# Performance work log

Measured on AMD Instinct MI355X. Metric: run time of the kernel, lower is better.

The kernel has to match this reference:

```python
import jax, jax.numpy as jnp
import numpy as np

HIDDEN = 1024
HEADS = 16
HEAD_DIM = HIDDEN // HEADS
SPARSITY_RATIO = 0.5


def setup_inputs() -> dict:
    key = jax.random.key(0)
    ks = jax.random.split(key, 6)
    B, S = 2, 2048
    # Xavier-uniform for square Linear weights: limit = sqrt(6/(fan_in+fan_out))
    lim = float(np.sqrt(6.0 / (HIDDEN + HIDDEN)))
    x = jax.random.normal(ks[0], (B, S, HIDDEN), dtype=jnp.float32)
    Wq = jax.random.uniform(ks[1], (HIDDEN, HIDDEN), minval=-lim, maxval=lim, dtype=jnp.float32)
    Wk = jax.random.uniform(ks[2], (HIDDEN, HIDDEN), minval=-lim, maxval=lim, dtype=jnp.float32)
    Wv = jax.random.uniform(ks[3], (HIDDEN, HIDDEN), minval=-lim, maxval=lim, dtype=jnp.float32)
    Wo = jax.random.uniform(ks[4], (HIDDEN, HIDDEN), minval=-lim, maxval=lim, dtype=jnp.float32)
    bo = jnp.zeros((HIDDEN,), dtype=jnp.float32)
    adaptive_threshold = jnp.asarray(0.1, dtype=jnp.float32)
    return {"x": x, "Wq": Wq, "Wk": Wk, "Wv": Wv, "Wo": Wo, "bo": bo,
            "adaptive_threshold": adaptive_threshold}


def reference(x, Wq, Wk, Wv, Wo, bo, adaptive_threshold):
    B, S, _ = x.shape
    H, D = HEADS, HEAD_DIM
    # projections (torch Linear: y = x @ W.T), split heads -> [B, H, S, D]
    q = (x @ Wq.T).reshape(B, S, H, D).transpose(0, 2, 1, 3)
    k = (x @ Wk.T).reshape(B, S, H, D).transpose(0, 2, 1, 3)
    v = (x @ Wv.T).reshape(B, S, H, D).transpose(0, 2, 1, 3)
    scores = jnp.einsum('bhqd,bhkd->bhqk', q, k) / jnp.sqrt(jnp.asarray(D, x.dtype))
    # adaptive top-k sparsity: keep top k entries per query row
    k_keep = max(1, int(S * (1.0 - SPARSITY_RATIO)))
    topv = jax.lax.top_k(scores, k_keep)[0]          # [B,H,S,k]
    kth = topv[..., -1:]                              # k-th largest per row
    thr = jnp.clip(adaptive_threshold, 0.0, 1.0)
    keep = (scores >= kth) & (scores >= thr)
    neg_inf = jnp.asarray(-jnp.inf, scores.dtype)
    masked = jnp.where(keep, scores, neg_inf)
    attn = jax.nn.softmax(masked, axis=-1)            # dropout is no-op in eval
    out = jnp.einsum('bhqk,bhkd->bhqd', attn, v)      # [B,H,S,D]
    out = out.transpose(0, 2, 1, 3).reshape(B, S, H * D)
    return out @ Wo.T + bo
```

## Files before the change

kernel.cpp:

```cpp
#include <hip/hip_runtime.h>
#include <hip/hip_bf16.h>
#include <cstdint>
#include <cstddef>

#define HIDDEN 1024
#define HEADS  16
#define HDIM   64
#define BATCH  2
#define SEQ    2048
#define MTOT   (BATCH*SEQ)
#define KSEL   1024
#define QT     16

typedef __attribute__((ext_vector_type(8))) short bf16x8;
typedef __attribute__((ext_vector_type(4))) float f32x4;

__device__ __forceinline__ unsigned short f2bf_rne(float f) {
    unsigned u = __float_as_uint(f);
    u += 0x7fffu + ((u >> 16) & 1u);
    return (unsigned short)(u >> 16);
}
__device__ __forceinline__ float bf2f(unsigned short h) {
    return __uint_as_float(((unsigned)h) << 16);
}
__device__ __forceinline__ int score_bucket(float v) {
    int b = (int)floorf(__fmaf_rn(v, 32.0f, 256.0f));
    return min(511, max(0, b));
}
__device__ __forceinline__ void gl2lds16(const unsigned short* g, unsigned short* l) {
    __builtin_amdgcn_global_load_lds(
        (const __attribute__((address_space(1))) unsigned int*)g,
        (__attribute__((address_space(3))) unsigned int*)l, 16, 0, 0);
}

__global__ __launch_bounds__(256) void split_bf(
    const float* __restrict__ src, unsigned short* __restrict__ hi,
    unsigned short* __restrict__ lo, int n4)
{
    int i = blockIdx.x * 256 + threadIdx.x;
    if (i >= n4) return;
    float4 v = ((const float4*)src)[i];
    unsigned short h0 = f2bf_rne(v.x), h1 = f2bf_rne(v.y);
    unsigned short h2 = f2bf_rne(v.z), h3 = f2bf_rne(v.w);
    uint2 hv, lv;
    hv.x = (unsigned)h0 | ((unsigned)h1 << 16);
    hv.y = (unsigned)h2 | ((unsigned)h3 << 16);
    lv.x = (unsigned)f2bf_rne(v.x - bf2f(h0)) | ((unsigned)f2bf_rne(v.y - bf2f(h1)) << 16);
    lv.y = (unsigned)f2bf_rne(v.z - bf2f(h2)) | ((unsigned)f2bf_rne(v.w - bf2f(h3)) << 16);
    *(uint2*)(hi + (size_t)i * 4) = hv;
    *(uint2*)(lo + (size_t)i * 4) = lv;
}

__device__ __forceinline__ void gemm_mainloop(
    const unsigned short* __restrict__ Ah, const unsigned short* __restrict__ Al,
    const unsigned short* __restrict__ Bh, const unsigned short* __restrict__ Bl,
    int n0, int m0, unsigned short* lds, f32x4 acc[4][4])
{
    const int t = threadIdx.x;
    const int lane = t & 63;
    const int wid = t >> 6;
    const int wn = wid & 1, wm = wid >> 1;
    const int quad = lane >> 4, n16 = lane & 15;

    unsigned short* lAh = lds;
    unsigned short* lAl = lds + 4096;
    unsigned short* lBh = lds + 8192;
    unsigned short* lBl = lds + 12288;

    int rowp[2], cp[2];
#pragma unroll
    for (int p = 0; p < 2; ++p) {
        int cidx = p * 256 + t;
        rowp[p] = cidx >> 2;
        cp[p]   = (cidx & 3) ^ ((rowp[p] >> 1) & 3);
    }
    const int wbase = (t >> 6) * 64;

    int offA[4], offB[4];
#pragma unroll
    for (int i = 0; i < 4; ++i) {
        int ra = wn * 64 + i * 16 + n16;
        offA[i] = ra * 32 + (quad ^ ((ra >> 1) & 3)) * 8;
        int rb = wm * 64 + i * 16 + n16;
        offB[i] = rb * 32 + (quad ^ ((rb >> 1) & 3)) * 8;
    }

    for (int k0 = 0; k0 < HIDDEN; k0 += 32) {
        __syncthreads();
#pragma unroll
        for (int p = 0; p < 2; ++p) {
            const size_t aoff = (size_t)(n0 + rowp[p]) * HIDDEN + k0 + cp[p] * 8;
            const size_t boff = (size_t)(m0 + rowp[p]) * HIDDEN + k0 + cp[p] * 8;
            const int ldst = (p * 256 + wbase) * 8;
            gl2lds16(Ah + aoff, lAh + ldst);
            gl2lds16(Al + aoff, lAl + ldst);
            gl2lds16(Bh + boff, lBh + ldst);
            gl2lds16(Bl + boff, lBl + ldst);
        }
        __syncthreads();

        bf16x8 fah[4], fal[4], fbh[4], fbl[4];
#pragma unroll
        for (int i = 0; i < 4; ++i) {
            fah[i] = *(const bf16x8*)(lAh + offA[i]);
            fal[i] = *(const bf16x8*)(lAl + offA[i]);
            fbh[i] = *(const bf16x8*)(lBh + offB[i]);
            fbl[i] = *(const bf16x8*)(lBl + offB[i]);
        }
#pragma unroll
        for (int i = 0; i < 4; ++i)
#pragma unroll
            for (int j = 0; j < 4; ++j) {
                acc[i][j] = __builtin_amdgcn_mfma_f32_16x16x32_bf16(fah[i], fbh[j], acc[i][j], 0, 0, 0);
                acc[i][j] = __builtin_amdgcn_mfma_f32_16x16x32_bf16(fah[i], fbl[j], acc[i][j], 0, 0, 0);
                acc[i][j] = __builtin_amdgcn_mfma_f32_16x16x32_bf16(fal[i], fbh[j], acc[i][j], 0, 0, 0);
            }
    }
}

__global__ __launch_bounds__(256) void qkv_gemm(
    const unsigned short* __restrict__ xh, const unsigned short* __restrict__ xl,
    const unsigned short* __restrict__ Wsp,
    unsigned short* __restrict__ Qh, unsigned short* __restrict__ Ql,
    unsigned short* __restrict__ Kh, unsigned short* __restrict__ Kl,
    unsigned short* __restrict__ Vt)
{
    __shared__ __align__(16) unsigned short lds[16384];
    const int z = blockIdx.z;
    const unsigned short* Wh = Wsp + (size_t)z * 2097152;
    const unsigned short* Wl = Wh + 1048576;
    const int m0 = blockIdx.x * 128, n0 = blockIdx.y * 128;

    f32x4 acc[4][4];
#pragma unroll
    for (int i = 0; i < 4; ++i)
#pragma unroll
        for (int j = 0; j < 4; ++j) acc[i][j] = (f32x4){0.f, 0.f, 0.f, 0.f};

    gemm_mainloop(Wh, Wl, xh, xl, n0, m0, lds, acc);

    const int t = threadIdx.x;
    const int lane = t & 63, wid = t >> 6;
    const int wn = wid & 1, wm = wid >> 1;
    const int quad = lane >> 4, n16 = lane & 15;
    const float scale = (z == 0) ? 0.125f : 1.0f;

    if (z < 2) {
        unsigned short* oh = z ? Kh : Qh;
        unsigned short* ol = z ? Kl : Ql;
#pragma unroll
        for (int i = 0; i < 4; ++i)
#pragma unroll
            for (int j = 0; j < 4; ++j) {
                int m  = m0 + wm * 64 + j * 16 + n16;
                int nn = n0 + wn * 64 + i * 16 + quad * 4;
                int bb = m >> 11, ss = m & (SEQ - 1);
                int hh = nn >> 6, dd = nn & 63;
                size_t base = ((size_t)(bb * HEADS + hh) * SEQ + ss) * HDIM + dd;
                unsigned short h[4], l[4];
#pragma unroll
                for (int r = 0; r < 4; ++r) {
                    float v = acc[i][j][r] * scale;
                    h[r] = f2bf_rne(v);
                    l[r] = f2bf_rne(v - bf2f(h[r]));
                }
                uint2 hv, lv;
                hv.x = (unsigned)h[0] | ((unsigned)h[1] << 16);
                hv.y = (unsigned)h[2] | ((unsigned)h[3] << 16);
                lv.x = (unsigned)l[0] | ((unsigned)l[1] << 16);
                lv.y = (unsigned)l[2] | ((unsigned)l[3] << 16);
                *(uint2*)(oh + base) = hv;
                *(uint2*)(ol + base) = lv;
            }
    } else {
#pragma unroll
        for (int i = 0; i < 4; ++i)
#pragma unroll
            for (int j = 0; j < 4; ++j) {
                int m  = m0 + wm * 64 + j * 16 + n16;
                int bb = m >> 11, ss = m & (SEQ - 1);
#pragma unroll
                for (int r = 0; r < 4; ++r) {
                    int nn = n0 + wn * 64 + i * 16 + quad * 4 + r;
                    int hh = nn >> 6, dd = nn & 63;
                    Vt[((size_t)(bb * HEADS + hh) * HDIM + dd) * SEQ + ss] =
                        f2bf_rne(acc[i][j][r]);
                }
            }
    }
}

__global__ __launch_bounds__(256) void out_gemm(
    const unsigned short* __restrict__ Oh, const unsigned short* __restrict__ Ol,
    const unsigned short* __restrict__ Woh, const unsigned short* __restrict__ Wol,
    const float* __restrict__ bias, float* __restrict__ out)
{
    __shared__ __align__(16) unsigned short lds[16384];
    const int m0 = blockIdx.x * 128, n0 = blockIdx.y * 128;

    f32x4 acc[4][4];
#pragma unroll
    for (int i = 0; i < 4; ++i)
#pragma unroll
        for (int j = 0; j < 4; ++j) acc[i][j] = (f32x4){0.f, 0.f, 0.f, 0.f};

    gemm_mainloop(Woh, Wol, Oh, Ol, n0, m0, lds, acc);

    const int t = threadIdx.x;
    const int lane = t & 63, wid = t >> 6;
    const int wn = wid & 1, wm = wid >> 1;
    const int quad = lane >> 4, n16 = lane & 15;
#pragma unroll
    for (int i = 0; i < 4; ++i)
#pragma unroll
        for (int j = 0; j < 4; ++j) {
            int m  = m0 + wm * 64 + j * 16 + n16;
            int nn = n0 + wn * 64 + i * 16 + quad * 4;
            float4 v;
            v.x = acc[i][j][0] + bias[nn + 0];
            v.y = acc[i][j][1] + bias[nn + 1];
            v.z = acc[i][j][2] + bias[nn + 2];
            v.w = acc[i][j][3] + bias[nn + 3];
            *(float4*)&out[(size_t)m * HIDDEN + nn] = v;
        }
}

__global__ __launch_bounds__(256, 2) void attn_mfma(
    const unsigned short* __restrict__ Qh, const unsigned short* __restrict__ Ql,
    const unsigned short* __restrict__ Kh, const unsigned short* __restrict__ Kl,
    const unsigned short* __restrict__ Vt, const float* __restrict__ thrp,
    unsigned short* __restrict__ Oh, unsigned short* __restrict__ Ol)
{
    __shared__ __align__(16) unsigned char U[40960];
    __shared__ __align__(16) float cand[16][64];
    __shared__ __align__(16) float Olds[16][64];
    __shared__ float smax[4][16], ssum[4][16];
    __shared__ unsigned csum[16][16];
    __shared__ float gmax[16], gsum[16], cutv[16], cthr[16];
    __shared__ int bcut[16], resid[16];
    __shared__ unsigned ccnt[16];

    const int t = threadIdx.x;
    const int lane = t & 63, wid = t >> 6;
    const int g = lane >> 4, n16 = lane & 15;
    const int bh = blockIdx.x & 31;
    const int q0 = (blockIdx.x >> 5) * QT;
    const int row0 = g * 4;

    unsigned* hist = (unsigned*)U;
    unsigned short* Pw = (unsigned short*)(U + wid*10240);

    const size_t qoff = ((size_t)bh*SEQ + q0 + n16)*HDIM + g*8;
    bf16x8 aqh0 = *(const bf16x8*)(Qh + qoff);
    bf16x8 aqh1 = *(const bf16x8*)(Qh + qoff + 32);
    bf16x8 aql0 = *(const bf16x8*)(Ql + qoff);
    bf16x8 aql1 = *(const bf16x8*)(Ql + qoff + 32);

    const unsigned short* khb = Kh + (size_t)bh*SEQ*HDIM;
    const unsigned short* klb = Kl + (size_t)bh*SEQ*HDIM;

    f32x4 sc[32];
#pragma unroll
    for (int tt = 0; tt < 32; ++tt) {
        const size_t kb = ((size_t)(wid*512 + tt*16 + n16))*HDIM + g*8;
        bf16x8 bh0 = *(const bf16x8*)(khb + kb);
        bf16x8 bh1 = *(const bf16x8*)(khb + kb + 32);
        bf16x8 bl0 = *(const bf16x8*)(klb + kb);
        bf16x8 bl1 = *(const bf16x8*)(klb + kb + 32);
        f32x4 a = {0.f, 0.f, 0.f, 0.f};
        a = __builtin_amdgcn_mfma_f32_16x16x32_bf16(aqh0, bh0, a, 0, 0, 0);
        a = __builtin_amdgcn_mfma_f32_16x16x32_bf16(aqh1, bh1, a, 0, 0, 0);
        a = __builtin_amdgcn_mfma_f32_16x16x32_bf16(aqh0, bl0, a, 0, 0, 0);
        a = __builtin_amdgcn_mfma_f32_16x16x32_bf16(aqh1, bl1, a, 0, 0, 0);
        a = __builtin_amdgcn_mfma_f32_16x16x32_bf16(aql0, bh0, a, 0, 0, 0);
        a = __builtin_amdgcn_mfma_f32_16x16x32_bf16(aql1, bh1, a, 0, 0, 0);
        sc[tt] = a;
    }

    for (int j = t; j < 16*513; j += 256) hist[j] = 0u;
    for (int j = t; j < 16*64; j += 256) ((float*)Olds)[j] = 0.f;
    if (t < 16) ccnt[t] = 0u;

    float rmax[4];
#pragma unroll
    for (int r = 0; r < 4; ++r) {
        float v = sc[0][r];
#pragma unroll
        for (int tt = 1; tt < 32; ++tt) v = fmaxf(v, sc[tt][r]);
#pragma unroll
        for (int m = 1; m < 16; m <<= 1) v = fmaxf(v, __shfl_xor(v, m));
        rmax[r] = v;
    }
    if (n16 == 0) {
#pragma unroll
        for (int r = 0; r < 4; ++r) smax[wid][row0 + r] = rmax[r];
    }
    __syncthreads();
    if (t < 16) gmax[t] = fmaxf(fmaxf(smax[0][t], smax[1][t]),
                                fmaxf(smax[2][t], smax[3][t]));

#pragma unroll
    for (int tt = 0; tt < 32; ++tt)
#pragma unroll
        for (int r = 0; r < 4; ++r) {
            int b = score_bucket(sc[tt][r]);
            atomicAdd(&hist[(row0 + r)*513 + b], 1u);
        }
    __syncthreads();

    {
        int row = t >> 4, slot = t & 15;
        int btop = 512 - slot*32;
        unsigned s = 0;
        for (int b = btop - 32; b < btop; ++b) s += hist[row*513 + b];
        csum[row][slot] = s;
    }
    __syncthreads();
    {
        int row = t >> 4, slot = t & 15;
        unsigned cum = 0;
        for (int j = 0; j < slot; ++j) cum += csum[row][j];
        unsigned cs = csum[row][slot];
        if (cum < (unsigned)KSEL && cum + cs >= (unsigned)KSEL) {
            unsigned c2 = cum;
            for (int b = 512 - slot*32 - 1; b >= 512 - (slot+1)*32; --b) {
                unsigned hb = hist[row*513 + b];
                if (c2 + hb >= (unsigned)KSEL) { bcut[row] = b; resid[row] = KSEL - (int)c2; break; }
                c2 += hb;
            }
        }
    }
    __syncthreads();
    if (t < 16) cutv[t] = ((float)bcut[t] - 256.0f) * 0.03125f;

#pragma unroll
    for (int tt = 0; tt < 32; ++tt)
#pragma unroll
        for (int r = 0; r < 4; ++r) {
            float v = sc[tt][r];
            int row = row0 + r;
            if (score_bucket(v) == bcut[row]) {
                unsigned idx = atomicAdd(&ccnt[row], 1u);
                if (idx < 64u) cand[row][idx] = v;
            }
        }
    __syncthreads();

    {
        int row = t >> 4, slot = t & 15;
        int n = min((int)ccnt[row], 64);
        int r = resid[row];
        for (int i = slot; i < n; i += 16) {
            float c = cand[row][i];
            int gt = 0, ge = 0;
            for (int j = 0; j < n; ++j) {
                float x = cand[row][j];
                gt += (x > c); ge += (x >= c);
            }
            if (gt < r && ge >= r) cutv[row] = c;
        }
    }
    __syncthreads();
    if (t < 16) {
        float th = fminf(fmaxf(thrp[0], 0.f), 1.f);
        cthr[t] = fmaxf(cutv[t], th);
    }
    __syncthreads();

    float mrow[4], crow[4], lsum[4];
#pragma unroll
    for (int r = 0; r < 4; ++r) {
        mrow[r] = gmax[row0 + r]; crow[r] = cthr[row0 + r]; lsum[r] = 0.f;
    }
#pragma unroll
    for (int tt = 0; tt < 32; ++tt)
#pragma unroll
        for (int r = 0; r < 4; ++r) {
            float v = sc[tt][r];
            float p = (v >= crow[r]) ? __expf(v - mrow[r]) : 0.f;
            sc[tt][r] = p;
            lsum[r] += p;
        }
#pragma unroll
    for (int r = 0; r < 4; ++r) {
#pragma unroll
        for (int m = 1; m < 16; m <<= 1) lsum[r] += __shfl_xor(lsum[r], m);
    }
    if (n16 == 0) {
#pragma unroll
        for (int r = 0; r < 4; ++r) ssum[wid][row0 + r] = lsum[r];
    }
    __syncthreads();
    if (t < 16) gsum[t] = ssum[0][t] + ssum[1][t] + ssum[2][t] + ssum[3][t];

    f32x4 oacc[4];
#pragma unroll
    for (int dt = 0; dt < 4; ++dt) oacc[dt] = (f32x4){0.f, 0.f, 0.f, 0.f};
    const unsigned short* vtb = Vt + (size_t)bh*HDIM*SEQ;

#pragma unroll
    for (int half = 0; half < 2; ++half) {
        __syncthreads();
#pragma unroll
        for (int tt2 = 0; tt2 < 16; ++tt2) {
            int tt = half*16 + tt2;
            int c = tt2*16 + n16;
            unsigned pk0 = (unsigned)f2bf_rne(sc[tt][0]) | ((unsigned)f2bf_rne(sc[tt][1]) << 16);
            unsigned pk1 = (unsigned)f2bf_rne(sc[tt][2]) | ((unsigned)f2bf_rne(sc[tt][3]) << 16);
            uint2 pk; pk.x = pk0; pk.y = pk1;
            *(uint2*)(Pw + (size_t)c*20 + row0) = pk;
        }
        __syncthreads();
#pragma unroll
        for (int kc = 0; kc < 8; ++kc) {
            bf16x8 af;
#pragma unroll
            for (int j = 0; j < 8; ++j)
                af[j] = ((const short*)Pw)[(kc*32 + g*8 + j)*20 + n16];
            const int sbase = wid*512 + half*256 + kc*32 + g*8;
#pragma unroll
            for (int dt = 0; dt < 4; ++dt) {
                const size_t vb = ((size_t)(dt*16 + n16))*SEQ + sbase;
                bf16x8 bf = *(const bf16x8*)(vtb + vb);
                oacc[dt] = __builtin_amdgcn_mfma_f32_16x16x32_bf16(af, bf, oacc[dt], 0, 0, 0);
            }
        }
    }

    __syncthreads();
#pragma unroll
    for (int dt = 0; dt < 4; ++dt)
#pragma unroll
        for (int r = 0; r < 4; ++r)
            atomicAdd(&Olds[row0 + r][dt*16 + n16], oacc[dt][r]);
    __syncthreads();
    {
        int row = t >> 4, d4 = (t & 15) * 4;
        float inv = 1.0f / gsum[row];
        float o0 = Olds[row][d4+0] * inv, o1 = Olds[row][d4+1] * inv;
        float o2 = Olds[row][d4+2] * inv, o3 = Olds[row][d4+3] * inv;
        unsigned short h0 = f2bf_rne(o0), h1 = f2bf_rne(o1);
        unsigned short h2 = f2bf_rne(o2), h3 = f2bf_rne(o3);
        uint2 hv, lv;
        hv.x = (unsigned)h0 | ((unsigned)h1 << 16);
        hv.y = (unsigned)h2 | ((unsigned)h3 << 16);
        lv.x = (unsigned)f2bf_rne(o0 - bf2f(h0)) | ((unsigned)f2bf_rne(o1 - bf2f(h1)) << 16);
        lv.y = (unsigned)f2bf_rne(o2 - bf2f(h2)) | ((unsigned)f2bf_rne(o3 - bf2f(h3)) << 16);
        const int bb = bh >> 4, hh = bh & 15;
        size_t base = ((size_t)(bb*SEQ + q0 + row))*HIDDEN + hh*HDIM + d4;
        *(uint2*)(Oh + base) = hv;
        *(uint2*)(Ol + base) = lv;
    }
}

extern "C" void kernel_launch(void* const* d_in, const int* in_sizes, int n_in,
                              void* d_out, int out_size, void* d_ws, size_t ws_size,
                              hipStream_t stream)
{
    (void)in_sizes; (void)n_in; (void)out_size; (void)ws_size;
    const float* x  = (const float*)d_in[0];
    const float* Wq = (const float*)d_in[1];
    const float* Wk = (const float*)d_in[2];
    const float* Wv = (const float*)d_in[3];
    const float* Wo = (const float*)d_in[4];
    const float* bo = (const float*)d_in[5];
    const float* at = (const float*)d_in[6];
    float* out = (float*)d_out;

    char* ws = (char*)d_ws;
    const size_t MB = 1048576;
    unsigned short* xh  = (unsigned short*)(ws);
    unsigned short* xl  = (unsigned short*)(ws + 8*MB);
    unsigned short* Wsp = (unsigned short*)(ws + 16*MB);
    unsigned short* Qh  = (unsigned short*)(ws + 32*MB);
    unsigned short* Ql  = (unsigned short*)(ws + 40*MB);
    unsigned short* Kh  = (unsigned short*)(ws + 48*MB);
    unsigned short* Kl  = (unsigned short*)(ws + 56*MB);
    unsigned short* Vt  = (unsigned short*)d_out;

    split_bf<<<MTOT*HIDDEN/4/256, 256, 0, stream>>>(x,  xh, xl, MTOT*HIDDEN/4);
    split_bf<<<HIDDEN*HIDDEN/4/256, 256, 0, stream>>>(Wq, Wsp + 0u*1048576u, Wsp + 1u*1048576u, HIDDEN*HIDDEN/4);
    split_bf<<<HIDDEN*HIDDEN/4/256, 256, 0, stream>>>(Wk, Wsp + 2u*1048576u, Wsp + 3u*1048576u, HIDDEN*HIDDEN/4);
    split_bf<<<HIDDEN*HIDDEN/4/256, 256, 0, stream>>>(Wv, Wsp + 4u*1048576u, Wsp + 5u*1048576u, HIDDEN*HIDDEN/4);
    split_bf<<<HIDDEN*HIDDEN/4/256, 256, 0, stream>>>(Wo, Wsp + 6u*1048576u, Wsp + 7u*1048576u, HIDDEN*HIDDEN/4);

    qkv_gemm<<<dim3(MTOT/128, HIDDEN/128, 3), 256, 0, stream>>>(xh, xl, Wsp, Qh, Ql, Kh, Kl, Vt);
    attn_mfma<<<BATCH*HEADS*(SEQ/QT), 256, 0, stream>>>(Qh, Ql, Kh, Kl, Vt, at, xh, xl);
    out_gemm<<<dim3(MTOT/128, HIDDEN/128, 1), 256, 0, stream>>>(xh, xl, Wsp + 6u*1048576u, Wsp + 7u*1048576u, bo, out);
}
```

Measured before the change: 795.2 us.

## Raise attention occupancy, shrink LDS, vectorize P reads and remap blocks

Result: slower. 1.031 ms (+29.7%).

```diff
diff --git a/kernel.cpp b/kernel.cpp
--- a/kernel.cpp
+++ b/kernel.cpp
@@ -225,32 +225,38 @@
         }
 }
 
-__global__ __launch_bounds__(256, 2) void attn_mfma(
+__global__ __launch_bounds__(256, 3) void attn_mfma(
     const unsigned short* __restrict__ Qh, const unsigned short* __restrict__ Ql,
     const unsigned short* __restrict__ Kh, const unsigned short* __restrict__ Kl,
     const unsigned short* __restrict__ Vt, const float* __restrict__ thrp,
     unsigned short* __restrict__ Oh, unsigned short* __restrict__ Ol)
 {
-    __shared__ __align__(16) unsigned char U[40960];
+    __shared__ __align__(16) unsigned char U[33792];
     __shared__ __align__(16) float cand[16][64];
     __shared__ __align__(16) float Olds[16][64];
     __shared__ float smax[4][16], ssum[4][16];
     __shared__ unsigned csum[16][16];
-    __shared__ float gmax[16], gsum[16], cutv[16], cthr[16];
+    __shared__ float gmax[16], gsum[16], cutv[16];
     __shared__ int bcut[16], resid[16];
     __shared__ unsigned ccnt[16];
 
     const int t = threadIdx.x;
     const int lane = t & 63, wid = t >> 6;
-    const int g = lane >> 4, n16 = lane & 15;
-    const int bh = blockIdx.x & 31;
-    const int q0 = (blockIdx.x >> 5) * QT;
-    const int row0 = g * 4;
+    const int quad = lane >> 4, n16 = lane & 15;
+    const int bh = (blockIdx.x & 7) + 8 * (int)(blockIdx.x >> 10);
+    const int q0 = ((blockIdx.x >> 3) & 127) * QT;
+    const int row0 = quad * 4;
 
     unsigned* hist = (unsigned*)U;
-    unsigned short* Pw = (unsigned short*)(U + wid*10240);
-
-    const size_t qoff = ((size_t)bh*SEQ + q0 + n16)*HDIM + g*8;
+    unsigned short* Pw = (unsigned short*)(U + wid * 8448);
+
+    const float thv = fminf(fmaxf(thrp[0], 0.f), 1.f);
+
+    for (int j = t; j < 16*513; j += 256) hist[j] = 0u;
+    for (int j = t; j < 16*64; j += 256) ((float*)Olds)[j] = 0.f;
+    if (t < 16) ccnt[t] = 0u;
+
+    const size_t qoff = ((size_t)bh*SEQ + q0 + n16)*HDIM + quad*8;
     bf16x8 aqh0 = *(const bf16x8*)(Qh + qoff);
     bf16x8 aqh1 = *(const bf16x8*)(Qh + qoff + 32);
     bf16x8 aql0 = *(const bf16x8*)(Ql + qoff);
@@ -262,7 +268,7 @@
     f32x4 sc[32];
 #pragma unroll
     for (int tt = 0; tt < 32; ++tt) {
-        const size_t kb = ((size_t)(wid*512 + tt*16 + n16))*HDIM + g*8;
+        const size_t kb = ((size_t)(wid*512 + tt*16 + n16))*HDIM + quad*8;
         bf16x8 bh0 = *(const bf16x8*)(khb + kb);
         bf16x8 bh1 = *(const bf16x8*)(khb + kb + 32);
         bf16x8 bl0 = *(const bf16x8*)(klb + kb);
@@ -277,10 +283,6 @@
         sc[tt] = a;
     }
 
-    for (int j = t; j < 16*513; j += 256) hist[j] = 0u;
-    for (int j = t; j < 16*64; j += 256) ((float*)Olds)[j] = 0.f;
-    if (t < 16) ccnt[t] = 0u;
-
     float rmax[4];
 #pragma unroll
     for (int r = 0; r < 4; ++r) {
@@ -316,22 +318,33 @@
         csum[row][slot] = s;
     }
     __syncthreads();
-    {
-        int row = t >> 4, slot = t & 15;
-        unsigned cum = 0;
-        for (int j = 0; j < slot; ++j) cum += csum[row][j];
-        unsigned cs = csum[row][slot];
-        if (cum < (unsigned)KSEL && cum + cs >= (unsigned)KSEL) {
-            unsigned c2 = cum;
-            for (int b = 512 - slot*32 - 1; b >= 512 - (slot+1)*32; --b) {
-                unsigned hb = hist[row*513 + b];
-                if (c2 + hb >= (unsigned)KSEL) { bcut[row] = b; resid[row] = KSEL - (int)c2; break; }
-                c2 += hb;
-            }
-        }
-    }
-    __syncthreads();
-    if (t < 16) cutv[t] = ((float)bcut[t] - 256.0f) * 0.03125f;
+
+    if (t < 16) {
+        unsigned cs[16];
+#pragma unroll
+        for (int j = 0; j < 16; ++j) cs[j] = csum[t][j];
+        unsigned cum = 0; int jc = -1;
+#pragma unroll
+        for (int j = 0; j < 16; ++j) {
+            bool here = (jc < 0) && (cum + cs[j] >= (unsigned)KSEL);
+            if (here) jc = j;
+            if (jc < 0) cum += cs[j];
+        }
+        int btop = 512 - jc*32;
+        unsigned hb[32];
+#pragma unroll
+        for (int i = 0; i < 32; ++i) hb[i] = hist[t*513 + btop - 1 - i];
+        unsigned c2 = cum; int bsel = btop - 32; int rres = 1; bool found = false;
+#pragma unroll
+        for (int i = 0; i < 32; ++i) {
+            bool here = !found && (c2 + hb[i] >= (unsigned)KSEL);
+            if (here) { bsel = btop - 1 - i; rres = KSEL - (int)c2; found = true; }
+            if (!found) c2 += hb[i];
+        }
+        bcut[t] = bsel; resid[t] = rres;
+        cutv[t] = ((float)bsel - 256.0f) * 0.03125f;
+    }
+    __syncthreads();
 
 #pragma unroll
     for (int tt = 0; tt < 32; ++tt)
@@ -361,34 +374,35 @@
         }
     }
     __syncthreads();
-    if (t < 16) {
-        float th = fminf(fmaxf(thrp[0], 0.f), 1.f);
-        cthr[t] = fmaxf(cutv[t], th);
-    }
-    __syncthreads();
-
-    float mrow[4], crow[4], lsum[4];
+
+    float mrow[4], crow[4], l4[4];
 #pragma unroll
     for (int r = 0; r < 4; ++r) {
-        mrow[r] = gmax[row0 + r]; crow[r] = cthr[row0 + r]; lsum[r] = 0.f;
-    }
-#pragma unroll
-    for (int tt = 0; tt < 32; ++tt)
+        mrow[r] = gmax[row0 + r];
+        crow[r] = fmaxf(cutv[row0 + r], thv);
+        l4[r] = 0.f;
+    }
+    unsigned pr01[32], pr23[32];
+#pragma unroll
+    for (int tt = 0; tt < 32; ++tt) {
+        float p[4];
 #pragma unroll
         for (int r = 0; r < 4; ++r) {
             float v = sc[tt][r];
-            float p = (v >= crow[r]) ? __expf(v - mrow[r]) : 0.f;
-            sc[tt][r] = p;
-            lsum[r] += p;
-        }
+            p[r] = (v >= crow[r]) ? __expf(v - mrow[r]) : 0.f;
+            l4[r] += p[r];
+        }
+        pr01[tt] = (unsigned)f2bf_rne(p[0]) | ((unsigned)f2bf_rne(p[1]) << 16);
+        pr23[tt] = (unsigned)f2bf_rne(p[2]) | ((unsigned)f2bf_rne(p[3]) << 16);
+    }
 #pragma unroll
     for (int r = 0; r < 4; ++r) {
 #pragma unroll
-        for (int m = 1; m < 16; m <<= 1) lsum[r] += __shfl_xor(lsum[r], m);
+        for (int m = 1; m < 16; m <<= 1) l4[r] += __shfl_xor(l4[r], m);
     }
     if (n16 == 0) {
 #pragma unroll
-        for (int r = 0; r < 4; ++r) ssum[wid][row0 + r] = lsum[r];
+        for (int r = 0; r < 4; ++r) ssum[wid][row0 + r] = l4[r];
     }
     __syncthreads();
     if (t < 16) gsum[t] = ssum[0][t] + ssum[1][t] + ssum[2][t] + ssum[3][t];
@@ -400,24 +414,19 @@
 
 #pragma unroll
     for (int half = 0; half < 2; ++half) {
-        __syncthreads();
 #pragma unroll
         for (int tt2 = 0; tt2 < 16; ++tt2) {
             int tt = half*16 + tt2;
-            int c = tt2*16 + n16;
-            unsigned pk0 = (unsigned)f2bf_rne(sc[tt][0]) | ((unsigned)f2bf_rne(sc[tt][1]) << 16);
-            unsigned pk1 = (unsigned)f2bf_rne(sc[tt][2]) | ((unsigned)f2bf_rne(sc[tt][3]) << 16);
-            uint2 pk; pk.x = pk0; pk.y = pk1;
-            *(uint2*)(Pw + (size_t)c*20 + row0) = pk;
-        }
-        __syncthreads();
+            int kl = tt2*16 + n16;
+            Pw[(row0 + 0)*264 + kl] = (unsigned short)(pr01[tt] & 0xffffu);
+            Pw[(row0 + 1)*264 + kl] = (unsigned short)(pr01[tt] >> 16);
+            Pw[(row0 + 2)*264 + kl] = (unsigned short)(pr23[tt] & 0xffffu);
+            Pw[(row0 + 3)*264 + kl] = (unsigned short)(pr23[tt] >> 16);
+        }
 #pragma unroll
         for (int kc = 0; kc < 8; ++kc) {
-            bf16x8 af;
-#pragma unroll
-            for (int j = 0; j < 8; ++j)
-                af[j] = ((const short*)Pw)[(kc*32 + g*8 + j)*20 + n16];
-            const int sbase = wid*512 + half*256 + kc*32 + g*8;
+            bf16x8 af = *(const bf16x8*)(Pw + n16*264 + kc*32 + quad*8);
+            const int sbase = wid*512 + half*256 + kc*32 + quad*8;
 #pragma unroll
             for (int dt = 0; dt < 4; ++dt) {
                 const size_t vb = ((size_t)(dt*16 + n16))*SEQ + sbase;
@@ -427,7 +436,6 @@
         }
     }
 
-    __syncthreads();
 #pragma unroll
     for (int dt = 0; dt < 4; ++dt)
 #pragma unroll
```
